# Kernel optimization log

Hardware: AMD Instinct MI355X
Metric: run time of the kernel (lower is better)

The kernel has to match this reference:

```python
import jax, jax.numpy as jnp
import numpy as np

N = 100000
E = 3200000
D_IN = 128
D_OUT = 128
EPS = 1e-5


def setup_inputs() -> dict:
    key = jax.random.key(0)
    ks = jax.random.split(key, 8)
    x = jax.random.normal(ks[0], (N, D_IN), dtype=jnp.float32)
    edge_index = jax.random.randint(ks[1], (2, E), 0, N, dtype=jnp.int32)
    # SAGEConv params: lin_l (neighbor path, has bias), lin_r (root path, no bias)
    s = 1.0 / np.sqrt(D_IN)
    W_l = jax.random.uniform(ks[2], (D_IN, D_OUT), jnp.float32, -s, s)
    b_l = jax.random.uniform(ks[3], (D_OUT,), jnp.float32, -s, s)
    W_r = jax.random.uniform(ks[4], (D_IN, D_OUT), jnp.float32, -s, s)
    # LayerNorm params
    gamma = jnp.ones((D_OUT,), jnp.float32)
    beta = jnp.zeros((D_OUT,), jnp.float32)
    return {"x": x, "edge_index": edge_index, "W_l": W_l, "b_l": b_l,
            "W_r": W_r, "gamma": gamma, "beta": beta}


def reference(x, edge_index, W_l, b_l, W_r, gamma, beta):
    src = edge_index[0]  # message sources
    dst = edge_index[1]  # aggregation targets
    n = x.shape[0]
    # mean aggregation over in-neighbors (SAGEConv default aggr='mean')
    summed = jax.ops.segment_sum(x[src], dst, num_segments=n)  # [N, D_IN]
    deg = jax.ops.segment_sum(jnp.ones((src.shape[0],), x.dtype), dst,
                              num_segments=n)
    mean_neigh = summed / jnp.maximum(deg, 1.0)[:, None]
    # SAGEConv: lin_l(mean_neigh) + lin_r(x)
    h = mean_neigh @ W_l + b_l + x @ W_r  # [N, D_OUT]
    # LayerNorm over last dim
    mu = jnp.mean(h, axis=-1, keepdims=True)
    var = jnp.mean(jnp.square(h - mu), axis=-1, keepdims=True)
    h = (h - mu) * jax.lax.rsqrt(var + EPS) * gamma + beta
    # exact (erf-based) GELU, matching torch nn.GELU default
    return jax.nn.gelu(h, approximate=False)
```

## Files before the change

kernel.cpp:

```cpp
#include <hip/hip_runtime.h>
#include <cstdint>
#include <cstddef>

#define NN 100000
#define NE 3200000
#define D 128

#define NBUK  1563
#define NBUKP 2048
#define BCAP  2560
#define EPB   12800
#define PBLK  250
#define CBLK  3125

typedef __attribute__((ext_vector_type(8))) short bf16x8;
typedef __attribute__((ext_vector_type(4))) float f32x4;
typedef __attribute__((ext_vector_type(2))) float f32x2;

__device__ __forceinline__ unsigned short f2bf(float f) {
    unsigned int u = __float_as_uint(f);
    u += 0x7FFFu + ((u >> 16) & 1u);
    return (unsigned short)(u >> 16);
}

__device__ __forceinline__ bf16x8 fp8x8_to_bf16x8(unsigned int lo, unsigned int hi) {
    const f32x2 p0 = __builtin_amdgcn_cvt_pk_f32_fp8(lo, false);
    const f32x2 p1 = __builtin_amdgcn_cvt_pk_f32_fp8(lo, true);
    const f32x2 p2 = __builtin_amdgcn_cvt_pk_f32_fp8(hi, false);
    const f32x2 p3 = __builtin_amdgcn_cvt_pk_f32_fp8(hi, true);
    union { unsigned int w[4]; bf16x8 v; } r;
    r.w[0] = (unsigned)f2bf(p0[0]) | ((unsigned)f2bf(p0[1]) << 16);
    r.w[1] = (unsigned)f2bf(p1[0]) | ((unsigned)f2bf(p1[1]) << 16);
    r.w[2] = (unsigned)f2bf(p2[0]) | ((unsigned)f2bf(p2[1]) << 16);
    r.w[3] = (unsigned)f2bf(p3[0]) | ((unsigned)f2bf(p3[1]) << 16);
    return r.v;
}

__global__ __launch_bounds__(512)
void k_all(const float* __restrict__ x,
           const int* __restrict__ ei,
           const float* __restrict__ Wl, const float* __restrict__ Wr,
           unsigned short* __restrict__ xb,
           unsigned char* __restrict__ xq,
           unsigned short* __restrict__ wf,
           unsigned int* __restrict__ gcur,
           unsigned int* __restrict__ ebuf)
{
    const int blk = blockIdx.x;
    const int t   = threadIdx.x;

    if (blk >= PBLK) {
        if (blk < PBLK + CBLK) {
            const size_t i8 = ((size_t)(blk - PBLK) * 512 + t) * 8;
            const float4 v0 = *reinterpret_cast<const float4*>(x + i8);
            const float4 v1 = *reinterpret_cast<const float4*>(x + i8 + 4);
            uint4 o;
            o.x = (unsigned)f2bf(v0.x) | ((unsigned)f2bf(v0.y) << 16);
            o.y = (unsigned)f2bf(v0.z) | ((unsigned)f2bf(v0.w) << 16);
            o.z = (unsigned)f2bf(v1.x) | ((unsigned)f2bf(v1.y) << 16);
            o.w = (unsigned)f2bf(v1.z) | ((unsigned)f2bf(v1.w) << 16);
            *reinterpret_cast<uint4*>(xb + i8) = o;
            int p0 = __builtin_amdgcn_cvt_pk_fp8_f32(v0.x, v0.y, 0, false);
            p0     = __builtin_amdgcn_cvt_pk_fp8_f32(v0.z, v0.w, p0, true);
            int p1 = __builtin_amdgcn_cvt_pk_fp8_f32(v1.x, v1.y, 0, false);
            p1     = __builtin_amdgcn_cvt_pk_fp8_f32(v1.z, v1.w, p1, true);
            uint2 q; q.x = (unsigned)p0; q.y = (unsigned)p1;
            *reinterpret_cast<uint2*>(xq + i8) = q;
        } else {
            const int tid  = (blk - PBLK - CBLK) * 512 + t;
            const int j    = tid & 7;
            const int lane = (tid >> 3) & 63;
            const int tt   = (tid >> 9) & 7;
            const int kt   = tid >> 12;
            const int k    = kt * 32 + (lane >> 4) * 8 + j;
            const int cc   = tt * 16 + (lane & 15);
            const float v  = (k < D) ? Wl[k * D + cc] : Wr[(k - D) * D + cc];
            wf[tid] = f2bf(v);
        }
        return;
    }

    __shared__ unsigned int staging[EPB];
    __shared__ unsigned int hist[NBUKP];
    __shared__ unsigned int partials[512];

    const int e0 = blk * EPB;

    #pragma unroll
    for (int k = 0; k < 4; ++k) hist[t * 4 + k] = 0u;
    __syncthreads();

    #pragma unroll
    for (int j = 0; j < 25; ++j) {
        const int d = ei[NE + e0 + j * 512 + t];
        atomicAdd(&hist[d >> 6], 1u);
    }
    __syncthreads();

    unsigned int c = 0;
    #pragma unroll
    for (int k = 0; k < 4; ++k) c += hist[t * 4 + k];
    partials[t] = c;
    __syncthreads();
    for (int dstep = 1; dstep < 512; dstep <<= 1) {
        const unsigned int v = (t >= dstep) ? partials[t - dstep] : 0u;
        __syncthreads();
        partials[t] += v;
        __syncthreads();
    }
    unsigned int running = (t == 0) ? 0u : partials[t - 1];
    #pragma unroll
    for (int k = 0; k < 4; ++k) {
        running += hist[t * 4 + k];
        hist[t * 4 + k] = running;
    }
    __syncthreads();

    #pragma unroll
    for (int j = 0; j < 25; ++j) {
        const int e = e0 + j * 512 + t;
        const int s = ei[e];
        const int d = ei[NE + e];
        const unsigned int pos = atomicSub(&hist[d >> 6], 1u) - 1u;
        staging[pos] = ((unsigned)(d & 63) << 17) | (unsigned)s;
    }
    __syncthreads();

    int i = t * 25;
    const int wEnd = i + 25;
    int lo = 0, hi = NBUKP - 1;
    while (lo < hi) {
        const int mid = (lo + hi + 1) >> 1;
        if ((int)hist[mid] <= i) lo = mid; else hi = mid - 1;
    }
    int bp = lo;
    while (i < wEnd) {
        while (bp + 1 < NBUKP && (int)hist[bp + 1] <= i) ++bp;
        const int bEnd = (bp + 1 < NBUKP) ? (int)hist[bp + 1] : EPB;
        const int runEnd = (wEnd < bEnd) ? wEnd : bEnd;
        const int len = runEnd - i;
        const unsigned int g = atomicAdd(&gcur[bp], (unsigned)len);
        if (g + (unsigned)len <= (unsigned)BCAP) {
            unsigned int dj = (unsigned)bp * BCAP + g;
            int k = 0;
            if ((dj & 1u) && k < len) { ebuf[dj] = staging[i + k]; ++k; ++dj; }
            for (; k + 1 < len; k += 2, dj += 2) {
                uint2 p; p.x = staging[i + k]; p.y = staging[i + k + 1];
                *reinterpret_cast<uint2*>(&ebuf[dj]) = p;
            }
            if (k < len) ebuf[dj] = staging[i + k];
        }
        i = runEnd;
    }
}

__global__ __launch_bounds__(256, 6)
void k_gather(const unsigned char* __restrict__ xq,
              const unsigned int* __restrict__ gcur,
              unsigned int* __restrict__ ebuf)
{
    __shared__ unsigned int ew[BCAP];
    __shared__ unsigned int hcnt[64];
    __shared__ unsigned int hstart[65];

    const int t    = threadIdx.x;
    const int w    = t >> 6;
    const int lane = t & 63;
    const int b    = blockIdx.x;

    const unsigned int cntu = gcur[b];
    const int count = (int)(cntu < (unsigned)BCAP ? cntu : (unsigned)BCAP);
    const size_t bb = (size_t)b * BCAP;

    unsigned int wreg[10];
    #pragma unroll
    for (int k = 0; k < 10; ++k) {
        const int i = t + k * 256;
        wreg[k] = (i < count) ? ebuf[bb + i] : 0xFFFFFFFFu;
    }
    if (t < 64) hcnt[t] = 0u;
    __syncthreads();

    #pragma unroll
    for (int k = 0; k < 10; ++k)
        if (wreg[k] != 0xFFFFFFFFu) atomicAdd(&hcnt[wreg[k] >> 17], 1u);
    __syncthreads();

    if (t < 64) {
        unsigned int p = hcnt[t];
        #pragma unroll
        for (int d = 1; d < 64; d <<= 1) {
            const unsigned int v = __shfl_up(p, d, 64);
            if (lane >= d) p += v;
        }
        hstart[t + 1] = p;
        if (t == 0) hstart[0] = 0u;
    }
    __syncthreads();
    if (t < 64) hcnt[t] = hstart[t];
    __syncthreads();

    #pragma unroll
    for (int k = 0; k < 10; ++k) {
        const unsigned int wv = wreg[k];
        if (wv != 0xFFFFFFFFu) {
            const unsigned int pos = atomicAdd(&hcnt[wv >> 17], 1u);
            ew[pos] = wv;
        }
    }
    __syncthreads();

    const int half = lane >> 5;
    const int hl   = lane & 31;
    const size_t boff = (size_t)(hl << 2);

    for (int i = 0; i < 16; ++i) {
        const int n = w * 16 + i;
        const int s = (int)hstart[n];
        const int e = (int)hstart[n + 1];
        const int dg = e - s;
        float a0 = 0.f, a1 = 0.f, a2 = 0.f, a3 = 0.f;
        int c = s;
        for (; c + 8 <= e; c += 8) {
            unsigned int u[4];
            #pragma unroll
            for (int j = 0; j < 4; ++j) {
                const unsigned int wj = ew[c + 2 * j + half];
                u[j] = *reinterpret_cast<const unsigned int*>(
                    xq + ((size_t)(wj & 0x1FFFFu) << 7) + boff);
            }
            #pragma unroll
            for (int j = 0; j < 4; ++j) {
                const f32x2 p = __builtin_amdgcn_cvt_pk_f32_fp8(u[j], false);
                const f32x2 q = __builtin_amdgcn_cvt_pk_f32_fp8(u[j], true);
                a0 += p[0]; a1 += p[1]; a2 += q[0]; a3 += q[1];
            }
        }
        for (; c + 2 <= e; c += 2) {
            const unsigned int w0 = ew[c + half];
            const unsigned int u0 = *reinterpret_cast<const unsigned int*>(
                xq + ((size_t)(w0 & 0x1FFFFu) << 7) + boff);
            const f32x2 p = __builtin_amdgcn_cvt_pk_f32_fp8(u0, false);
            const f32x2 q = __builtin_amdgcn_cvt_pk_f32_fp8(u0, true);
            a0 += p[0]; a1 += p[1]; a2 += q[0]; a3 += q[1];
        }
        if (c < e && half == 0) {
            const unsigned int w0 = ew[c];
            const unsigned int u0 = *reinterpret_cast<const unsigned int*>(
                xq + ((size_t)(w0 & 0x1FFFFu) << 7) + boff);
            const f32x2 p = __builtin_amdgcn_cvt_pk_f32_fp8(u0, false);
            const f32x2 q = __builtin_amdgcn_cvt_pk_f32_fp8(u0, true);
            a0 += p[0]; a1 += p[1]; a2 += q[0]; a3 += q[1];
        }
        a0 += __shfl_xor(a0, 32, 64);
        a1 += __shfl_xor(a1, 32, 64);
        a2 += __shfl_xor(a2, 32, 64);
        a3 += __shfl_xor(a3, 32, 64);
        const float inv = 1.0f / (float)(dg > 1 ? dg : 1);
        if (half == 0) {
            int pk = __builtin_amdgcn_cvt_pk_fp8_f32(a0 * inv, a1 * inv, 0, false);
            pk     = __builtin_amdgcn_cvt_pk_fp8_f32(a2 * inv, a3 * inv, pk, true);
            ebuf[bb + (unsigned)(n << 5) + (unsigned)hl] = (unsigned)pk;
        }
    }
}

__global__ __launch_bounds__(256)
void k_gemm(const unsigned short* __restrict__ xb,
            const unsigned int* __restrict__ ebuf,
            const unsigned short* __restrict__ wf,
            const float* __restrict__ bl,
            const float* __restrict__ gamma,
            const float* __restrict__ beta,
            float* __restrict__ out)
{
    __shared__ unsigned char smean[64][136];

    const int t    = threadIdx.x;
    const int w    = t >> 6;
    const int lane = t & 63;
    const int b    = blockIdx.x;
    const int nodeBase = b * 64;

    const unsigned int* gm = ebuf + (size_t)b * BCAP;
    #pragma unroll
    for (int k = 0; k < 8; ++k) {
        const int idx = k * 256 + t;
        const int row = idx >> 5;
        const int c4  = (idx & 31) << 2;
        *reinterpret_cast<unsigned int*>(&smean[row][c4]) = gm[idx];
    }
    __syncthreads();

    const int row  = lane & 15;
    const int kgrp = lane >> 4;
    const int node_r = nodeBase + w * 16 + row;
    const size_t xrow = (size_t)(node_r < NN ? node_r : NN - 1) << 7;

    f32x4 accr[8];
    const f32x4 zero = {0.f, 0.f, 0.f, 0.f};
    #pragma unroll
    for (int q = 0; q < 8; ++q) accr[q] = zero;

    #pragma unroll
    for (int kt = 0; kt < 8; ++kt) {
        bf16x8 a;
        if (kt < 4) {
            const uint2 m8 = *reinterpret_cast<const uint2*>(
                &smean[w * 16 + row][kt * 32 + kgrp * 8]);
            a = fp8x8_to_bf16x8(m8.x, m8.y);
        } else {
            a = *reinterpret_cast<const bf16x8*>(xb + xrow + (kt - 4) * 32 + kgrp * 8);
        }
        #pragma unroll
        for (int q = 0; q < 8; ++q) {
            const bf16x8 bfrag = *reinterpret_cast<const bf16x8*>(
                wf + (((kt * 8 + q) * 64 + lane) << 3));
            accr[q] = __builtin_amdgcn_mfma_f32_16x16x32_bf16(a, bfrag, accr[q], 0, 0, 0);
        }
    }

    const int col = lane & 15;
    float gv[8], bev[8], blv[8];
    #pragma unroll
    for (int q = 0; q < 8; ++q) {
        gv[q]  = gamma[q * 16 + col];
        bev[q] = beta[q * 16 + col];
        blv[q] = bl[q * 16 + col];
    }
    const float k2 = 0.70710678118654752f;
    #pragma unroll
    for (int r = 0; r < 4; ++r) {
        float p = 0.f, p2 = 0.f;
        #pragma unroll
        for (int q = 0; q < 8; ++q) {
            const float h = accr[q][r] + blv[q];
            p += h; p2 += h * h;
        }
        #pragma unroll
        for (int m = 1; m <= 8; m <<= 1) {
            p  += __shfl_xor(p,  m, 64);
            p2 += __shfl_xor(p2, m, 64);
        }
        const float mu   = p * (1.0f / 128.0f);
        const float var  = p2 * (1.0f / 128.0f) - mu * mu;
        const float rstd = rsqrtf(var + 1e-5f);
        const int node = nodeBase + w * 16 + kgrp * 4 + r;
        if (node < NN) {
            #pragma unroll
            for (int q = 0; q < 8; ++q) {
                const float h = accr[q][r] + blv[q];
                const float y = (h - mu) * rstd * gv[q] + bev[q];
                out[(size_t)node * D + q * 16 + col] = 0.5f * y * (1.0f + erff(y * k2));
            }
        }
    }
}

extern "C" void kernel_launch(void* const* d_in, const int* in_sizes, int n_in,
                              void* d_out, int out_size, void* d_ws, size_t ws_size,
                              hipStream_t stream)
{
    const float* x     = (const float*)d_in[0];
    const int*   ei    = (const int*)d_in[1];
    const float* Wl    = (const float*)d_in[2];
    const float* bl    = (const float*)d_in[3];
    const float* Wr    = (const float*)d_in[4];
    const float* gamma = (const float*)d_in[5];
    const float* beta  = (const float*)d_in[6];
    float* out = (float*)d_out;

    char* wsp = (char*)d_ws;
    unsigned int*   gcur = (unsigned int*)(wsp + 0);
    unsigned int*   ebuf = (unsigned int*)(wsp + 32768);
    unsigned short* xb   = (unsigned short*)(wsp + 16416768);
    unsigned char*  xq   = (unsigned char*)(wsp + 42016768);
    unsigned short* wf   = (unsigned short*)(wsp + 54816768);

    hipMemsetAsync(gcur, 0, NBUKP * sizeof(unsigned int), stream);

    k_all<<<PBLK + CBLK + 64, 512, 0, stream>>>(x, ei, Wl, Wr, xb, xq, wf,
                                                gcur, ebuf);

    k_gather<<<NBUK, 256, 0, stream>>>(xq, gcur, ebuf);

    k_gemm<<<NBUK, 256, 0, stream>>>(xb, ebuf, wf, bl, gamma, beta, out);
}
```

Measured before the change: 157.4 us.

## Drop bf16 copy of x, convert in GEMM; widen prep blocks to 1024 threads

The bf16 copy of x is no longer written in the prep kernel. The GEMM now reads fp32 x directly and converts it to bf16 in registers, which removes a 25.6MB write plus its later read in exchange for reading 51MB of fp32 in the GEMM. The prep/bucketing kernel also moves to 1024-thread blocks, and destination indices are kept in registers between the histogram and scatter passes so they are not reloaded. The scan now runs over 1024 partials, which means more synchronization steps, and occupancy may drop.

```diff
diff --git a/kernel.cpp b/kernel.cpp
--- a/kernel.cpp
+++ b/kernel.cpp
@@ -11,7 +11,7 @@
 #define BCAP  2560
 #define EPB   12800
 #define PBLK  250
-#define CBLK  3125
+#define CBLK  1563
 
 typedef __attribute__((ext_vector_type(8))) short bf16x8;
 typedef __attribute__((ext_vector_type(4))) float f32x4;
@@ -36,11 +36,10 @@
     return r.v;
 }
 
-__global__ __launch_bounds__(512)
+__global__ __launch_bounds__(1024)
 void k_all(const float* __restrict__ x,
            const int* __restrict__ ei,
            const float* __restrict__ Wl, const float* __restrict__ Wr,
-           unsigned short* __restrict__ xb,
            unsigned char* __restrict__ xq,
            unsigned short* __restrict__ wf,
            unsigned int* __restrict__ gcur,
@@ -51,23 +50,19 @@
 
     if (blk >= PBLK) {
         if (blk < PBLK + CBLK) {
-            const size_t i8 = ((size_t)(blk - PBLK) * 512 + t) * 8;
-            const float4 v0 = *reinterpret_cast<const float4*>(x + i8);
-            const float4 v1 = *reinterpret_cast<const float4*>(x + i8 + 4);
-            uint4 o;
-            o.x = (unsigned)f2bf(v0.x) | ((unsigned)f2bf(v0.y) << 16);
-            o.y = (unsigned)f2bf(v0.z) | ((unsigned)f2bf(v0.w) << 16);
-            o.z = (unsigned)f2bf(v1.x) | ((unsigned)f2bf(v1.y) << 16);
-            o.w = (unsigned)f2bf(v1.z) | ((unsigned)f2bf(v1.w) << 16);
-            *reinterpret_cast<uint4*>(xb + i8) = o;
-            int p0 = __builtin_amdgcn_cvt_pk_fp8_f32(v0.x, v0.y, 0, false);
-            p0     = __builtin_amdgcn_cvt_pk_fp8_f32(v0.z, v0.w, p0, true);
-            int p1 = __builtin_amdgcn_cvt_pk_fp8_f32(v1.x, v1.y, 0, false);
-            p1     = __builtin_amdgcn_cvt_pk_fp8_f32(v1.z, v1.w, p1, true);
-            uint2 q; q.x = (unsigned)p0; q.y = (unsigned)p1;
-            *reinterpret_cast<uint2*>(xq + i8) = q;
+            const size_t i8 = ((size_t)(blk - PBLK) * 1024 + t) * 8;
+            if (i8 < (size_t)NN * D) {
+                const float4 v0 = *reinterpret_cast<const float4*>(x + i8);
+                const float4 v1 = *reinterpret_cast<const float4*>(x + i8 + 4);
+                int p0 = __builtin_amdgcn_cvt_pk_fp8_f32(v0.x, v0.y, 0, false);
+                p0     = __builtin_amdgcn_cvt_pk_fp8_f32(v0.z, v0.w, p0, true);
+                int p1 = __builtin_amdgcn_cvt_pk_fp8_f32(v1.x, v1.y, 0, false);
+                p1     = __builtin_amdgcn_cvt_pk_fp8_f32(v1.z, v1.w, p1, true);
+                uint2 q; q.x = (unsigned)p0; q.y = (unsigned)p1;
+                *reinterpret_cast<uint2*>(xq + i8) = q;
+            }
         } else {
-            const int tid  = (blk - PBLK - CBLK) * 512 + t;
+            const int tid  = (blk - PBLK - CBLK) * 1024 + t;
             const int j    = tid & 7;
             const int lane = (tid >> 3) & 63;
             const int tt   = (tid >> 9) & 7;
@@ -82,27 +77,28 @@
 
     __shared__ unsigned int staging[EPB];
     __shared__ unsigned int hist[NBUKP];
-    __shared__ unsigned int partials[512];
+    __shared__ unsigned int partials[1024];
 
     const int e0 = blk * EPB;
 
-    #pragma unroll
-    for (int k = 0; k < 4; ++k) hist[t * 4 + k] = 0u;
-    __syncthreads();
-
-    #pragma unroll
-    for (int j = 0; j < 25; ++j) {
-        const int d = ei[NE + e0 + j * 512 + t];
-        atomicAdd(&hist[d >> 6], 1u);
-    }
-    __syncthreads();
-
-    unsigned int c = 0;
-    #pragma unroll
-    for (int k = 0; k < 4; ++k) c += hist[t * 4 + k];
+    hist[t] = 0u; hist[t + 1024] = 0u;
+    __syncthreads();
+
+    int dreg[13];
+    #pragma unroll
+    for (int j = 0; j < 13; ++j) {
+        const int e = j * 1024 + t;
+        if (e < EPB) {
+            dreg[j] = ei[NE + e0 + e];
+            atomicAdd(&hist[dreg[j] >> 6], 1u);
+        }
+    }
+    __syncthreads();
+
+    unsigned int c = hist[t * 2] + hist[t * 2 + 1];
     partials[t] = c;
     __syncthreads();
-    for (int dstep = 1; dstep < 512; dstep <<= 1) {
+    for (int dstep = 1; dstep < 1024; dstep <<= 1) {
         const unsigned int v = (t >= dstep) ? partials[t - dstep] : 0u;
         __syncthreads();
         partials[t] += v;
@@ -110,24 +106,26 @@
     }
     unsigned int running = (t == 0) ? 0u : partials[t - 1];
     #pragma unroll
-    for (int k = 0; k < 4; ++k) {
-        running += hist[t * 4 + k];
-        hist[t * 4 + k] = running;
-    }
-    __syncthreads();
-
-    #pragma unroll
-    for (int j = 0; j < 25; ++j) {
-        const int e = e0 + j * 512 + t;
-        const int s = ei[e];
-        const int d = ei[NE + e];
-        const unsigned int pos = atomicSub(&hist[d >> 6], 1u) - 1u;
-        staging[pos] = ((unsigned)(d & 63) << 17) | (unsigned)s;
-    }
-    __syncthreads();
-
-    int i = t * 25;
-    const int wEnd = i + 25;
+    for (int k = 0; k < 2; ++k) {
+        running += hist[t * 2 + k];
+        hist[t * 2 + k] = running;
+    }
+    __syncthreads();
+
+    #pragma unroll
+    for (int j = 0; j < 13; ++j) {
+        const int e = j * 1024 + t;
+        if (e < EPB) {
+            const int s = ei[e0 + e];
+            const int d = dreg[j];
+            const unsigned int pos = atomicSub(&hist[d >> 6], 1u) - 1u;
+            staging[pos] = ((unsigned)(d & 63) << 17) | (unsigned)s;
+        }
+    }
+    __syncthreads();
+
+    int i = (t * 25) >> 1;
+    const int wEnd = ((t + 1) * 25) >> 1;
     int lo = 0, hi = NBUKP - 1;
     while (lo < hi) {
         const int mid = (lo + hi + 1) >> 1;
@@ -266,7 +264,7 @@
 }
 
 __global__ __launch_bounds__(256)
-void k_gemm(const unsigned short* __restrict__ xb,
+void k_gemm(const float* __restrict__ x,
             const unsigned int* __restrict__ ebuf,
             const unsigned short* __restrict__ wf,
             const float* __restrict__ bl,
@@ -295,7 +293,7 @@
     const int row  = lane & 15;
     const int kgrp = lane >> 4;
     const int node_r = nodeBase + w * 16 + row;
-    const size_t xrow = (size_t)(node_r < NN ? node_r : NN - 1) << 7;
+    const float* xp = x + ((size_t)(node_r < NN ? node_r : NN - 1) << 7);
 
     f32x4 accr[8];
     const f32x4 zero = {0.f, 0.f, 0.f, 0.f};
@@ -310,7 +308,16 @@
                 &smean[w * 16 + row][kt * 32 + kgrp * 8]);
             a = fp8x8_to_bf16x8(m8.x, m8.y);
         } else {
-            a = *reinterpret_cast<const bf16x8*>(xb + xrow + (kt - 4) * 32 + kgrp * 8);
+            const float4 va = *reinterpret_cast<const float4*>(
+                xp + (kt - 4) * 32 + kgrp * 8);
+            const float4 vb = *reinterpret_cast<const float4*>(
+                xp + (kt - 4) * 32 + kgrp * 8 + 4);
+            union { unsigned int wd[4]; bf16x8 v; } r;
+            r.wd[0] = (unsigned)f2bf(va.x) | ((unsigned)f2bf(va.y) << 16);
+            r.wd[1] = (unsigned)f2bf(va.z) | ((unsigned)f2bf(va.w) << 16);
+            r.wd[2] = (unsigned)f2bf(vb.x) | ((unsigned)f2bf(vb.y) << 16);
+            r.wd[3] = (unsigned)f2bf(vb.z) | ((unsigned)f2bf(vb.w) << 16);
+            a = r.v;
         }
         #pragma unroll
         for (int q = 0; q < 8; ++q) {
@@ -373,16 +380,15 @@
     char* wsp = (char*)d_ws;
     unsigned int*   gcur = (unsigned int*)(wsp + 0);
     unsigned int*   ebuf = (unsigned int*)(wsp + 32768);
-    unsigned short* xb   = (unsigned short*)(wsp + 16416768);
-    unsigned char*  xq   = (unsigned char*)(wsp + 42016768);
-    unsigned short* wf   = (unsigned short*)(wsp + 54816768);
+    unsigned char*  xq   = (unsigned char*)(wsp + 16037888);
+    unsigned short* wf   = (unsigned short*)(wsp + 28837888);
 
     hipMemsetAsync(gcur, 0, NBUKP * sizeof(unsigned int), stream);
 
-    k_all<<<PBLK + CBLK + 64, 512, 0, stream>>>(x, ei, Wl, Wr, xb, xq, wf,
-                                                gcur, ebuf);
+    k_all<<<PBLK + CBLK + 32, 1024, 0, stream>>>(x, ei, Wl, Wr, xq, wf,
+                                                 gcur, ebuf);
 
     k_gather<<<NBUK, 256, 0, stream>>>(xq, gcur, ebuf);
 
-    k_gemm<<<NBUK, 256, 0, stream>>>(xb, ebuf, wf, bl, gamma, beta, out);
-}
+    k_gemm<<<NBUK, 256, 0, stream>>>(x, ebuf, wf, bl, gamma, beta, out);
+}
```

Measured after the change: 148.9 us. 5.4% less time.
